# Performance work log

Measured on AMD Instinct MI355X. Metric: run time of the kernel, lower is better.

## Reference

```python
import jax, jax.numpy as jnp
import numpy as np

H = 16        # num_attention_heads
DH = 64       # attention_head_dim
D = H * DH    # model dim = 1024
FF = 4 * D    # feed-forward inner dim = 4096
SCALE = DH ** -0.5
EPS = 1e-12


def _ln(x, g, b):
    m = jnp.mean(x, axis=-1, keepdims=True)
    v = jnp.mean((x - m) ** 2, axis=-1, keepdims=True)
    return (x - m) * jax.lax.rsqrt(v + EPS) * g + b


def _attn(x, ctx, Wq, Wk, Wv, Wo, bo, mask):
    # x: [B,S,D] (already pre-normed), ctx: [B,T,D], mask: [B,T] int (1=keep) or None
    B, S, _ = x.shape
    T = ctx.shape[1]
    q = (x @ Wq).reshape(B, S, H, DH)
    k = (ctx @ Wk).reshape(B, T, H, DH)
    v = (ctx @ Wv).reshape(B, T, H, DH)
    scores = jnp.einsum('bqhd,bkhd->bhqk', q, k) * SCALE  # [B,H,S,T]
    if mask is not None:
        scores = jnp.where(mask[:, None, None, :] == 0, -jnp.inf, scores)
    probs = jax.nn.softmax(scores, axis=-1)
    out = jnp.einsum('bhqk,bkhd->bqhd', probs, v).reshape(B, S, D)
    return out @ Wo + bo


def _geglu_ff(x, Wff1, bff1, Wff2, bff2):
    y = x @ Wff1 + bff1                 # [B,S,2*FF]
    h, gate = y[..., :FF], y[..., FF:]
    # GEGLU computes exact (erf) gelu in fp32
    g = jax.nn.gelu(gate.astype(jnp.float32), approximate=False).astype(gate.dtype)
    return (h * g) @ Wff2 + bff2


def setup_inputs() -> dict:
    key = jax.random.key(0)
    ks = jax.random.split(key, 24)
    B, S, T = 4, 1024, 1024
    w = lambda k, shp: jax.random.normal(k, shp, dtype=jnp.float32) * 0.02
    inp = {
        'hidden_states': jax.random.normal(ks[0], (B, S, D), dtype=jnp.float32),
        'context': jax.random.normal(ks[1], (B, T, D), dtype=jnp.float32),
        'encoder_key_padding_mask': jnp.ones((B, T), dtype=jnp.int32),
        'g1': jnp.ones((D,), jnp.float32), 'b1': jnp.zeros((D,), jnp.float32),
        'g2': jnp.ones((D,), jnp.float32), 'b2': jnp.zeros((D,), jnp.float32),
        'g3': jnp.ones((D,), jnp.float32), 'b3': jnp.zeros((D,), jnp.float32),
        'Wq1': w(ks[2], (D, D)), 'Wk1': w(ks[3], (D, D)), 'Wv1': w(ks[4], (D, D)),
        'Wo1': w(ks[5], (D, D)), 'bo1': jnp.zeros((D,), jnp.float32),
        'Wq2': w(ks[6], (D, D)), 'Wk2': w(ks[7], (D, D)), 'Wv2': w(ks[8], (D, D)),
        'Wo2': w(ks[9], (D, D)), 'bo2': jnp.zeros((D,), jnp.float32),
        'Wff1': w(ks[10], (D, 2 * FF)), 'bff1': jnp.zeros((2 * FF,), jnp.float32),
        'Wff2': w(ks[11], (FF, D)), 'bff2': jnp.zeros((D,), jnp.float32),
    }
    return inp


def reference(hidden_states, context, encoder_key_padding_mask,
              g1, b1, g2, b2, g3, b3,
              Wq1, Wk1, Wv1, Wo1, bo1,
              Wq2, Wk2, Wv2, Wo2, bo2,
              Wff1, bff1, Wff2, bff2):
    # Self-attention (attn1): context defaults to (normed) hidden_states, no padding mask
    n1 = _ln(hidden_states, g1, b1)
    h = hidden_states + _attn(n1, n1, Wq1, Wk1, Wv1, Wo1, bo1, None)
    # Cross-attention (attn2) with encoder key padding mask
    n2 = _ln(h, g2, b2)
    h = h + _attn(n2, context, Wq2, Wk2, Wv2, Wo2, bo2, encoder_key_padding_mask)
    # GEGLU feed-forward
    h = h + _geglu_ff(_ln(h, g3, b3), Wff1, bff1, Wff2, bff2)
    return h
```

## Files before the change

### kernel.cpp

```cpp
#include <hip/hip_runtime.h>

typedef unsigned short u16;
typedef unsigned int u32;

#define B_ 4
#define S_ 1024
#define D_ 1024
#define H_ 16
#define DH_ 64
#define FF_ 4096
#define M_ 4096
#define SCALE_ 0.125f

typedef __attribute__((ext_vector_type(8))) __bf16 bf16x8;
typedef __attribute__((ext_vector_type(4))) float f32x4;

__device__ __forceinline__ f32x4 mfma16(bf16x8 a, bf16x8 b, f32x4 c) {
  return __builtin_amdgcn_mfma_f32_16x16x32_bf16(a, b, c, 0, 0, 0);
}

__device__ __forceinline__ u16 f2bf(float x) {
  union { __bf16 h; u16 u; } cv; cv.h = (__bf16)x; return cv.u;
}
__device__ __forceinline__ float bf2f(u16 u) {
  union { u32 u; float f; } cv; cv.u = ((u32)u) << 16; return cv.f;
}
__device__ __forceinline__ u32 packbf2(float a, float b) {
  union { u32 u; __bf16 h[2]; } pk;
  pk.h[0] = (__bf16)a; pk.h[1] = (__bf16)b;
  return pk.u;
}
__device__ __forceinline__ float gelu_exact(float x) {
  return 0.5f * x * (1.f + erff(x * 0.7071067811865475f));
}
__device__ __forceinline__ void gload16(const void* g, void* l) {
  __builtin_amdgcn_global_load_lds((__attribute__((address_space(1))) void*)(g),
                                   (__attribute__((address_space(3))) void*)(l),
                                   16, 0, 0);
}

template<int EPI>
__global__ __launch_bounds__(256, 2) void gemm128(
    const u16* __restrict__ A, const u16* __restrict__ BT,
    const float* __restrict__ bias, const float* __restrict__ res,
    const u16* __restrict__ aux, void* __restrict__ out,
    int M, int N, int K, int ktiles)
{
  __shared__ u16 As[2][128 * 64];
  __shared__ u16 Bs[2][128 * 64];

  const int tid = threadIdx.x;
  const int wave = tid >> 6, lane = tid & 63;
  const int wm = wave >> 1, wn = wave & 1;
  const int qi = lane & 15, g = lane >> 4;

  const int gx = N >> 7;
  const int nwg = gx * (M >> 7);
  int id = blockIdx.y * gridDim.x + blockIdx.x;
  id = (id & 7) * (nwg >> 3) + (id >> 3);
  const int m0 = (id / gx) << 7, n0 = (id % gx) << 7;

  const int NT = ktiles;
  const int kbase = blockIdx.z * ktiles * 64;

  const int r0 = tid >> 3;
  const int scol = (((tid & 7) ^ ((tid >> 3) & 7)) << 3);
  const int swb = wave << 6;

  f32x4 acc[4][4];
#pragma unroll
  for (int i = 0; i < 4; ++i)
#pragma unroll
    for (int j = 0; j < 4; ++j)
      acc[i][j] = (f32x4){0.f, 0.f, 0.f, 0.f};

#define STAGE_A(t, h, b) {                                                  \
    const int tt = (t) >= NT ? (t) - NT : (t);                              \
    _Pragma("unroll")                                                       \
    for (int i = 0; i < 2; ++i) {                                           \
      const int r = (h) * 64 + i * 32 + r0;                                 \
      gload16(A + (size_t)(m0 + r) * K + kbase + tt * 64 + scol,            \
              &As[b][(h) * 4096 + (i * 256 + swb) * 8]);                    \
    } }
#define STAGE_B(t, h, b) {                                                  \
    const int tt = (t) >= NT ? (t) - NT : (t);                              \
    _Pragma("unroll")                                                       \
    for (int i = 0; i < 2; ++i) {                                           \
      const int r = (h) * 64 + i * 32 + r0;                                 \
      gload16(BT + (size_t)(n0 + r) * K + kbase + tt * 64 + scol,           \
              &Bs[b][(h) * 4096 + (i * 256 + swb) * 8]);                    \
    } }

  bf16x8 af[4][2], bfr[4][2];

#define RD_ALL(b)                                                            \
  _Pragma("unroll") for (int mi = 0; mi < 4; ++mi)                           \
  _Pragma("unroll") for (int kk = 0; kk < 2; ++kk) {                         \
    const int row = wm * 64 + mi * 16 + qi;                                  \
    const int cb = ((kk * 64 + (g << 4)) ^ ((qi & 7) << 4));                 \
    af[mi][kk] = *(const bf16x8*)((const char*)&As[b][0] + row * 128 + cb);  \
  }                                                                          \
  _Pragma("unroll") for (int ni = 0; ni < 4; ++ni)                           \
  _Pragma("unroll") for (int kk = 0; kk < 2; ++kk) {                         \
    const int row = wn * 64 + ni * 16 + qi;                                  \
    const int cb = ((kk * 64 + (g << 4)) ^ ((qi & 7) << 4));                 \
    bfr[ni][kk] = *(const bf16x8*)((const char*)&Bs[b][0] + row * 128 + cb); \
  }

#define HALF(milo)                                                           \
  _Pragma("unroll") for (int mi = (milo); mi < (milo) + 2; ++mi)             \
  _Pragma("unroll") for (int ni = 0; ni < 4; ++ni)                           \
  _Pragma("unroll") for (int kk = 0; kk < 2; ++kk)                           \
    acc[mi][ni] = mfma16(af[mi][kk], bfr[ni][kk], acc[mi][ni]);

#define BAR() __builtin_amdgcn_s_barrier()
#define LGKM0() { asm volatile("s_waitcnt lgkmcnt(0)" ::: "memory");         \
                  __builtin_amdgcn_sched_barrier(0); }
#define VM8() asm volatile("s_waitcnt vmcnt(8)" ::: "memory")
#define PRIO(x) __builtin_amdgcn_s_setprio(x)

  STAGE_A(0, 0, 0); STAGE_A(0, 1, 0); STAGE_B(0, 0, 0); STAGE_B(0, 1, 0);
  STAGE_A(1, 0, 1); STAGE_A(1, 1, 1); STAGE_B(1, 0, 1); STAGE_B(1, 1, 1);
  VM8();
  BAR();

  const int NI = NT >> 1;
  for (int it = 0; it < NI; ++it) {
    const int k = it * 2;
    RD_ALL(0); LGKM0();
    BAR();
    STAGE_A(k + 2, 0, 0); STAGE_A(k + 2, 1, 0);
    PRIO(1); HALF(0); PRIO(0);
    STAGE_B(k + 2, 0, 0); STAGE_B(k + 2, 1, 0);
    PRIO(1); HALF(2); PRIO(0);
    VM8();
    BAR();
    RD_ALL(1); LGKM0();
    BAR();
    STAGE_A(k + 3, 0, 1); STAGE_A(k + 3, 1, 1);
    PRIO(1); HALF(0); PRIO(0);
    STAGE_B(k + 3, 0, 1); STAGE_B(k + 3, 1, 1);
    PRIO(1); HALF(2); PRIO(0);
    VM8();
    BAR();
  }

#pragma unroll
  for (int mi = 0; mi < 4; ++mi) {
#pragma unroll
    for (int ni = 0; ni < 4; ++ni) {
#pragma unroll
      for (int r = 0; r < 4; ++r) {
        const int m = m0 + wm * 64 + mi * 16 + g * 4 + r;
        const int n = n0 + wn * 64 + ni * 16 + qi;
        float v = acc[mi][ni][r];
        if (EPI == 0 || EPI == 5) {
          const int ts = n >> 10, b = m >> 10, s = m & 1023;
          const int hh = (n >> 6) & 15, dh = n & 63;
          if (EPI == 0 && ts == 0) v *= SCALE_;
          ((u16*)out)[(size_t)ts * (B_ * H_ * S_ * DH_) +
                      (((size_t)(b * H_ + hh) * S_) + s) * DH_ + dh] = f2bf(v);
        } else if (EPI == 1) {
          const size_t idx = (size_t)m * N + n;
          ((float*)out)[idx] = res[idx] + v + bias[n];
        } else if (EPI == 2) {
          ((u16*)out)[(size_t)m * N + n] = f2bf(gelu_exact(v + bias[n]));
        } else if (EPI == 3) {
          const size_t idx = (size_t)m * N + n;
          ((u16*)out)[idx] = f2bf((v + bias[n]) * bf2f(aux[idx]));
        } else {
          const size_t idx = (size_t)blockIdx.z * ((size_t)M * N) +
                             (size_t)m * N + n;
          ((u16*)out)[idx] = f2bf(v);
        }
      }
    }
  }
#undef STAGE_A
#undef STAGE_B
#undef RD_ALL
#undef HALF
#undef BAR
#undef LGKM0
#undef VM8
#undef PRIO
}

template<int EPI>
__global__ __launch_bounds__(512, 2) void gemm256b(
    const u16* __restrict__ A, const u16* __restrict__ BT,
    const float* __restrict__ bias, const float* __restrict__ res,
    const u16* __restrict__ aux, void* __restrict__ out,
    int M, int N, int K, int ktiles)
{
  __shared__ u16 As[2][256 * 64];
  __shared__ u16 Bs[2][256 * 64];

  const int tid = threadIdx.x;
  const int wave = tid >> 6, lane = tid & 63;
  const int wm = wave >> 2, wn = wave & 3;
  const int qi = lane & 15, g = lane >> 4;

  const int gx = N >> 8;
  const int nwg = gx * (M >> 8);
  int id = blockIdx.y * gridDim.x + blockIdx.x;
  id = (id & 7) * (nwg >> 3) + (id >> 3);
  const int m0 = (id / gx) << 8, n0 = (id % gx) << 8;

  const int NT = ktiles;
  const int kbase = blockIdx.z * ktiles * 64;

  const int srow = tid >> 3;
  const int scol = (((tid & 7) ^ ((tid >> 3) & 7)) << 3);
  const int sldsb = wave << 9;

  f32x4 acc[8][4];
#pragma unroll
  for (int i = 0; i < 8; ++i)
#pragma unroll
    for (int j = 0; j < 4; ++j)
      acc[i][j] = (f32x4){0.f, 0.f, 0.f, 0.f};

#define STAGE_A(t, b) {                                                     \
    const int tt = (t) >= NT ? (t) - NT : (t);                              \
    _Pragma("unroll")                                                       \
    for (int i = 0; i < 4; ++i) {                                           \
      const int r = i * 64 + srow;                                          \
      gload16(A + (size_t)(m0 + r) * K + kbase + tt * 64 + scol,            \
              &As[b][i * 4096 + sldsb]);                                    \
    } }
#define STAGE_B(t, b) {                                                     \
    const int tt = (t) >= NT ? (t) - NT : (t);                              \
    _Pragma("unroll")                                                       \
    for (int i = 0; i < 4; ++i) {                                           \
      const int r = i * 64 + srow;                                          \
      gload16(BT + (size_t)(n0 + r) * K + kbase + tt * 64 + scol,           \
              &Bs[b][i * 4096 + sldsb]);                                    \
    } }

  bf16x8 af[8][2], bfr[4][2];

#define RD_ALL(b)                                                            \
  _Pragma("unroll") for (int mi = 0; mi < 8; ++mi)                           \
  _Pragma("unroll") for (int kk = 0; kk < 2; ++kk) {                         \
    const int row = wm * 128 + mi * 16 + qi;                                 \
    const int cb = ((kk * 64 + (g << 4)) ^ ((qi & 7) << 4));                 \
    af[mi][kk] = *(const bf16x8*)((const char*)&As[b][0] + row * 128 + cb);  \
  }                                                                          \
  _Pragma("unroll") for (int ni = 0; ni < 4; ++ni)                           \
  _Pragma("unroll") for (int kk = 0; kk < 2; ++kk) {                         \
    const int row = wn * 64 + ni * 16 + qi;                                  \
    const int cb = ((kk * 64 + (g << 4)) ^ ((qi & 7) << 4));                 \
    bfr[ni][kk] = *(const bf16x8*)((const char*)&Bs[b][0] + row * 128 + cb); \
  }

#define MHALF(milo)                                                          \
  _Pragma("unroll") for (int mi = (milo); mi < (milo) + 4; ++mi)             \
  _Pragma("unroll") for (int ni = 0; ni < 4; ++ni)                           \
  _Pragma("unroll") for (int kk = 0; kk < 2; ++kk)                           \
    acc[mi][ni] = mfma16(af[mi][kk], bfr[ni][kk], acc[mi][ni]);

#define BAR() __builtin_amdgcn_s_barrier()
#define LGKM0() { asm volatile("s_waitcnt lgkmcnt(0)" ::: "memory");         \
                  __builtin_amdgcn_sched_barrier(0); }
#define VM8() asm volatile("s_waitcnt vmcnt(8)" ::: "memory")
#define PRIO(x) __builtin_amdgcn_s_setprio(x)

  STAGE_A(0, 0); STAGE_B(0, 0);
  STAGE_A(1, 1); STAGE_B(1, 1);
  VM8();
  BAR();

  for (int t = 0; t < NT; ++t) {
    const int b = t & 1;
    RD_ALL(b); LGKM0();
    BAR();
    STAGE_A(t + 2, b);
    PRIO(1); MHALF(0); PRIO(0);
    STAGE_B(t + 2, b);
    PRIO(1); MHALF(4); PRIO(0);
    VM8();
    BAR();
  }

#pragma unroll
  for (int mi = 0; mi < 8; ++mi) {
#pragma unroll
    for (int ni = 0; ni < 4; ++ni) {
#pragma unroll
      for (int r = 0; r < 4; ++r) {
        const int m = m0 + wm * 128 + mi * 16 + g * 4 + r;
        const int n = n0 + wn * 64 + ni * 16 + qi;
        const float v = acc[mi][ni][r];
        if (EPI == 2) {
          ((u16*)out)[(size_t)m * N + n] = f2bf(gelu_exact(v + bias[n]));
        } else if (EPI == 3) {
          const size_t idx = (size_t)m * N + n;
          ((u16*)out)[idx] = f2bf((v + bias[n]) * bf2f(aux[idx]));
        } else {
          const size_t idx = (size_t)blockIdx.z * ((size_t)M * N) +
                             (size_t)m * N + n;
          ((u16*)out)[idx] = f2bf(v);
        }
      }
    }
  }
#undef STAGE_A
#undef STAGE_B
#undef RD_ALL
#undef MHALF
#undef BAR
#undef LGKM0
#undef VM8
#undef PRIO
}

template<bool DOLN, int NS>
__global__ __launch_bounds__(256) void reduce_ln(
    const u16* __restrict__ p, const float* __restrict__ bias,
    const float* __restrict__ res, float* __restrict__ outf,
    const float* __restrict__ gg, const float* __restrict__ bb,
    u16* __restrict__ outn)
{
  __shared__ float red[8];
  const int row = blockIdx.x, tid = threadIdx.x;
  const size_t base = (size_t)row * 1024 + tid * 4;
  const size_t total = (size_t)M_ * 1024;
  float a0 = 0.f, a1 = 0.f, a2 = 0.f, a3 = 0.f;
#pragma unroll
  for (int s = 0; s < NS; ++s) {
    const uint2 u = *(const uint2*)&p[(size_t)s * total + base];
    a0 += bf2f((u16)(u.x & 0xffff));
    a1 += bf2f((u16)(u.x >> 16));
    a2 += bf2f((u16)(u.y & 0xffff));
    a3 += bf2f((u16)(u.y >> 16));
  }
  const float4 b4 = ((const float4*)bias)[tid];
  const float4 r4 = *(const float4*)&res[base];
  float4 o;
  o.x = r4.x + a0 + b4.x;
  o.y = r4.y + a1 + b4.y;
  o.z = r4.z + a2 + b4.z;
  o.w = r4.w + a3 + b4.w;
  *(float4*)&outf[base] = o;

  if (DOLN) {
    float s1 = o.x + o.y + o.z + o.w;
    float s2 = o.x * o.x + o.y * o.y + o.z * o.z + o.w * o.w;
#pragma unroll
    for (int m = 32; m; m >>= 1) {
      s1 += __shfl_xor(s1, m);
      s2 += __shfl_xor(s2, m);
    }
    const int wave = tid >> 6, lane = tid & 63;
    if (lane == 0) { red[wave * 2] = s1; red[wave * 2 + 1] = s2; }
    __syncthreads();
    const float St = red[0] + red[2] + red[4] + red[6];
    const float SQt = red[1] + red[3] + red[5] + red[7];
    const float mean = St * (1.f / 1024.f);
    float var = SQt * (1.f / 1024.f) - mean * mean;
    var = fmaxf(var, 0.f);
    const float rinv = rsqrtf(var + 1e-12f);
    const float4 g4 = ((const float4*)gg)[tid];
    const float4 bb4 = ((const float4*)bb)[tid];
    uint2 w;
    w.x = packbf2((o.x - mean) * rinv * g4.x + bb4.x,
                  (o.y - mean) * rinv * g4.y + bb4.y);
    w.y = packbf2((o.z - mean) * rinv * g4.z + bb4.z,
                  (o.w - mean) * rinv * g4.w + bb4.w);
    ((uint2*)(outn + (size_t)row * 1024))[tid] = w;
  }
}

template<int NS, bool QSC>
__global__ __launch_bounds__(256) void reduce_perm(
    const u16* __restrict__ p, u16* __restrict__ out, int M, int N)
{
  const size_t flat = ((size_t)blockIdx.x * 256 + threadIdx.x) * 4;
  const size_t total = (size_t)M * N;
  float a0 = 0.f, a1 = 0.f, a2 = 0.f, a3 = 0.f;
#pragma unroll
  for (int s = 0; s < NS; ++s) {
    const uint2 u = *(const uint2*)&p[(size_t)s * total + flat];
    a0 += bf2f((u16)(u.x & 0xffff));
    a1 += bf2f((u16)(u.x >> 16));
    a2 += bf2f((u16)(u.y & 0xffff));
    a3 += bf2f((u16)(u.y >> 16));
  }
  if (QSC) { a0 *= SCALE_; a1 *= SCALE_; a2 *= SCALE_; a3 *= SCALE_; }
  const int m = (int)(flat / N), nb = (int)(flat % N);
  const int ts = nb >> 10, hh = (nb >> 6) & 15, dh = nb & 63;
  const int b = m >> 10, sI = m & 1023;
  uint2 w;
  w.x = packbf2(a0, a1);
  w.y = packbf2(a2, a3);
  *(uint2*)&out[(size_t)ts * (B_ * H_ * S_ * DH_) +
                (((size_t)(b * H_ + hh) * S_) + sI) * DH_ + dh] = w;
}

template<bool MASKED>
__global__ __launch_bounds__(256, 4) void attn_kernel(
    const u16* __restrict__ Q, const u16* __restrict__ Kb,
    const u16* __restrict__ VT, const float* __restrict__ bias,
    u16* __restrict__ O, int S, int T)
{
  __shared__ u16 Ks[64 * 72];
  __shared__ u16 VTs[64 * 72];
  __shared__ u16 Ps[4][16 * 72];
  __shared__ float biasS[64];

  const int bh = blockIdx.y;
  const int b = bh >> 4, h = bh & 15;
  const int tid = threadIdx.x;
  const int wave = tid >> 6, lane = tid & 63;
  const int g = lane >> 4, qi = lane & 15;
  const int q0w = blockIdx.x * 64 + wave * 16;

  const u16* Qb = Q + (size_t)bh * S * DH_;
  const u16* Kg = Kb + (size_t)bh * T * DH_;
  const u16* Vg = VT + (size_t)bh * DH_ * T;

  bf16x8 qf[2];
  qf[0] = *(const bf16x8*)&Qb[(q0w + qi) * DH_ + g * 8];
  qf[1] = *(const bf16x8*)&Qb[(q0w + qi) * DH_ + 32 + g * 8];

  f32x4 acc[4];
#pragma unroll
  for (int i = 0; i < 4; ++i) acc[i] = (f32x4){0.f, 0.f, 0.f, 0.f};
  float l_run = 1e-30f;

  u16* Pw = &Ps[wave][0];

  for (int t0 = 0; t0 < T; t0 += 64) {
    __syncthreads();
#pragma unroll
    for (int i = 0; i < 2; ++i) {
      const int flat = i * 256 + tid;
      const int row = flat >> 3, kc = flat & 7;
      *(uint4*)&Ks[row * 72 + kc * 8] = *(const uint4*)&Kg[(size_t)(t0 + row) * DH_ + kc * 8];
      *(uint4*)&VTs[row * 72 + kc * 8] = *(const uint4*)&Vg[(size_t)row * T + t0 + kc * 8];
    }
    if (MASKED && tid < 64) biasS[tid] = bias[b * T + t0 + tid];
    __syncthreads();

    f32x4 sacc[4];
#pragma unroll
    for (int nt = 0; nt < 4; ++nt) sacc[nt] = (f32x4){0.f, 0.f, 0.f, 0.f};
#pragma unroll
    for (int kk = 0; kk < 2; ++kk) {
#pragma unroll
      for (int nt = 0; nt < 4; ++nt) {
        bf16x8 kf = *(const bf16x8*)&Ks[(nt * 16 + qi) * 72 + kk * 32 + g * 8];
        sacc[nt] = mfma16(kf, qf[kk], sacc[nt]);
      }
    }
    float p[4][4];
    float lsum = 0.f;
#pragma unroll
    for (int nt = 0; nt < 4; ++nt)
#pragma unroll
      for (int r = 0; r < 4; ++r) {
        float v = sacc[nt][r];
        if (MASKED) v += biasS[nt * 16 + g * 4 + r];
        const float e = __expf(v);
        p[nt][r] = e;
        lsum += e;
      }
    lsum += __shfl_xor(lsum, 16);
    lsum += __shfl_xor(lsum, 32);
    l_run += lsum;

#pragma unroll
    for (int nt = 0; nt < 4; ++nt) {
      uint2 w;
      w.x = packbf2(p[nt][0], p[nt][1]);
      w.y = packbf2(p[nt][2], p[nt][3]);
      *(uint2*)&Pw[qi * 72 + nt * 16 + g * 4] = w;
    }

#pragma unroll
    for (int kk = 0; kk < 2; ++kk) {
      bf16x8 pf = *(const bf16x8*)&Pw[qi * 72 + kk * 32 + g * 8];
#pragma unroll
      for (int ndh = 0; ndh < 4; ++ndh) {
        bf16x8 vf = *(const bf16x8*)&VTs[(ndh * 16 + qi) * 72 + kk * 32 + g * 8];
        acc[ndh] = mfma16(vf, pf, acc[ndh]);
      }
    }
  }

  const float inv = 1.f / l_run;
  const int qg = q0w + qi;
#pragma unroll
  for (int ndh = 0; ndh < 4; ++ndh) {
    uint2 w;
    w.x = packbf2(acc[ndh][0] * inv, acc[ndh][1] * inv);
    w.y = packbf2(acc[ndh][2] * inv, acc[ndh][3] * inv);
    *(uint2*)&O[(size_t)(b * S_ + qg) * D_ + h * DH_ + ndh * 16 + g * 4] = w;
  }
}

__global__ __launch_bounds__(256) void ln_kernel(
    const float* __restrict__ x, const float* __restrict__ gg,
    const float* __restrict__ bb, u16* __restrict__ out)
{
  __shared__ float red[8];
  const int row = blockIdx.x, tid = threadIdx.x;
  const float4 v = ((const float4*)(x + (size_t)row * D_))[tid];
  float s = v.x + v.y + v.z + v.w;
  float sq = v.x * v.x + v.y * v.y + v.z * v.z + v.w * v.w;
#pragma unroll
  for (int m = 32; m; m >>= 1) {
    s += __shfl_xor(s, m);
    sq += __shfl_xor(sq, m);
  }
  const int wave = tid >> 6, lane = tid & 63;
  if (lane == 0) { red[wave * 2] = s; red[wave * 2 + 1] = sq; }
  __syncthreads();
  const float St = red[0] + red[2] + red[4] + red[6];
  const float SQt = red[1] + red[3] + red[5] + red[7];
  const float mean = St * (1.f / 1024.f);
  float var = SQt * (1.f / 1024.f) - mean * mean;
  var = fmaxf(var, 0.f);
  const float rinv = rsqrtf(var + 1e-12f);
  const float4 g4 = ((const float4*)gg)[tid];
  const float4 b4 = ((const float4*)bb)[tid];
  uint2 o;
  o.x = packbf2((v.x - mean) * rinv * g4.x + b4.x, (v.y - mean) * rinv * g4.y + b4.y);
  o.y = packbf2((v.z - mean) * rinv * g4.z + b4.z, (v.w - mean) * rinv * g4.w + b4.w);
  ((uint2*)(out + (size_t)row * D_))[tid] = o;
}

__global__ __launch_bounds__(256) void transpose_w(
    const float* __restrict__ in, u16* __restrict__ out, int K, int N)
{
  __shared__ float tile[32][33];
  const int tx = threadIdx.x & 31, ty = threadIdx.x >> 5;
  const int k0 = blockIdx.y * 32, n0 = blockIdx.x * 32;
#pragma unroll
  for (int j = 0; j < 4; ++j)
    tile[ty + 8 * j][tx] = in[(size_t)(k0 + ty + 8 * j) * N + n0 + tx];
  __syncthreads();
#pragma unroll
  for (int j = 0; j < 4; ++j)
    out[(size_t)(n0 + ty + 8 * j) * K + k0 + tx] = f2bf(tile[tx][ty + 8 * j]);
}

__global__ __launch_bounds__(256) void transpose_v(
    const u16* __restrict__ in, u16* __restrict__ out, int T)
{
  __shared__ u16 tile[32][33];
  const int tx = threadIdx.x & 31, ty = threadIdx.x >> 5;
  const int bh = blockIdx.z;
  const int t0 = blockIdx.x * 32, d0 = blockIdx.y * 32;
  const u16* ib = in + (size_t)bh * T * DH_;
  u16* ob = out + (size_t)bh * DH_ * T;
#pragma unroll
  for (int j = 0; j < 4; ++j)
    tile[ty + 8 * j][tx] = ib[(size_t)(t0 + ty + 8 * j) * DH_ + d0 + tx];
  __syncthreads();
#pragma unroll
  for (int j = 0; j < 4; ++j)
    ob[(size_t)(d0 + ty + 8 * j) * T + t0 + tx] = tile[tx][ty + 8 * j];
}

__global__ void cvt_bf16(const float* __restrict__ in, u16* __restrict__ out, int n4)
{
  const int i = blockIdx.x * blockDim.x + threadIdx.x;
  if (i < n4) {
    const float4 v = ((const float4*)in)[i];
    uint2 o;
    o.x = packbf2(v.x, v.y);
    o.y = packbf2(v.z, v.w);
    ((uint2*)out)[i] = o;
  }
}

__global__ void mask_bias(const int* __restrict__ mask, float* __restrict__ bias, int n)
{
  const int i = blockIdx.x * blockDim.x + threadIdx.x;
  if (i < n) bias[i] = mask[i] ? 0.f : -1e30f;
}

extern "C" void kernel_launch(void* const* d_in, const int* in_sizes, int n_in,
                              void* d_out, int out_size, void* d_ws, size_t ws_size,
                              hipStream_t stream)
{
  (void)in_sizes; (void)n_in; (void)out_size; (void)ws_size;
  const float* hidden = (const float*)d_in[0];
  const float* ctx    = (const float*)d_in[1];
  const int*   mask   = (const int*)d_in[2];
  const float* g1 = (const float*)d_in[3];
  const float* b1 = (const float*)d_in[4];
  const float* g2 = (const float*)d_in[5];
  const float* b2 = (const float*)d_in[6];
  const float* g3 = (const float*)d_in[7];
  const float* b3 = (const float*)d_in[8];
  const float* Wq1 = (const float*)d_in[9];
  const float* Wk1 = (const float*)d_in[10];
  const float* Wv1 = (const float*)d_in[11];
  const float* Wo1 = (const float*)d_in[12];
  const float* bo1 = (const float*)d_in[13];
  const float* Wq2 = (const float*)d_in[14];
  const float* Wk2 = (const float*)d_in[15];
  const float* Wv2 = (const float*)d_in[16];
  const float* Wo2 = (const float*)d_in[17];
  const float* bo2 = (const float*)d_in[18];
  const float* Wff1 = (const float*)d_in[19];
  const float* bff1 = (const float*)d_in[20];
  const float* Wff2 = (const float*)d_in[21];
  const float* bff2 = (const float*)d_in[22];

  char* ws = (char*)d_ws;
  size_t off = 0;
  auto alloc = [&](size_t bytes) -> void* {
    void* p = ws + off;
    off += (bytes + 255) & ~(size_t)255;
    return p;
  };
  u16* WqT1  = (u16*)alloc((size_t)1024 * 1024 * 2);
  u16* WkT1  = (u16*)alloc((size_t)1024 * 1024 * 2);
  u16* WvT1  = (u16*)alloc((size_t)1024 * 1024 * 2);
  u16* WoT1  = (u16*)alloc((size_t)1024 * 1024 * 2);
  u16* WqT2  = (u16*)alloc((size_t)1024 * 1024 * 2);
  u16* WkT2  = (u16*)alloc((size_t)1024 * 1024 * 2);
  u16* WvT2  = (u16*)alloc((size_t)1024 * 1024 * 2);
  u16* WoT2  = (u16*)alloc((size_t)1024 * 1024 * 2);
  u16* Wff1T = (u16*)alloc((size_t)8192 * 1024 * 2);
  u16* Wff2T = (u16*)alloc((size_t)1024 * 4096 * 2);
  u16* nbuf  = (u16*)alloc((size_t)M_ * D_ * 2);
  u16* hgbuf = (u16*)alloc((size_t)M_ * FF_ * 2);
  u16* qbuf  = (u16*)alloc((size_t)M_ * D_ * 2);
  u16* kbuf  = (u16*)alloc((size_t)M_ * D_ * 2);
  u16* vbuf  = (u16*)alloc((size_t)M_ * D_ * 2);
  u16* vtbuf = (u16*)alloc((size_t)M_ * D_ * 2);
  u16* attnb = (u16*)alloc((size_t)M_ * D_ * 2);
  u16* ctxb  = (u16*)alloc((size_t)M_ * D_ * 2);
  u16* pbuf  = (u16*)alloc((size_t)4 * M_ * D_ * 2);
  float* biasw = (float*)alloc((size_t)B_ * S_ * 4);
  u16* gbuf = qbuf;
  float* hres = (float*)d_out;

  const dim3 blk(256);
  const dim3 blk512(512);
  const dim3 gW(32, 32);
  const dim3 gQKV(24, 32);
  const dim3 gKV(16, 32);
  const dim3 gFFb(16, 16);
  const dim3 gF2b(4, 16, 4);
  const dim3 gS2(8, 32, 2);
  const dim3 gA(16, 64);
  const dim3 gV(32, 2, 64);
  const dim3 gR(4096);

  transpose_w<<<gW, blk, 0, stream>>>(Wq1, WqT1, 1024, 1024);
  transpose_w<<<gW, blk, 0, stream>>>(Wk1, WkT1, 1024, 1024);
  transpose_w<<<gW, blk, 0, stream>>>(Wv1, WvT1, 1024, 1024);
  transpose_w<<<gW, blk, 0, stream>>>(Wo1, WoT1, 1024, 1024);
  transpose_w<<<gW, blk, 0, stream>>>(Wq2, WqT2, 1024, 1024);
  transpose_w<<<gW, blk, 0, stream>>>(Wk2, WkT2, 1024, 1024);
  transpose_w<<<gW, blk, 0, stream>>>(Wv2, WvT2, 1024, 1024);
  transpose_w<<<gW, blk, 0, stream>>>(Wo2, WoT2, 1024, 1024);
  transpose_w<<<dim3(256, 32), blk, 0, stream>>>(Wff1, Wff1T, 1024, 8192);
  transpose_w<<<dim3(32, 128), blk, 0, stream>>>(Wff2, Wff2T, 4096, 1024);
  cvt_bf16<<<dim3((1048576 + 255) / 256), blk, 0, stream>>>(ctx, ctxb, 1048576);
  mask_bias<<<dim3(16), blk, 0, stream>>>(mask, biasw, B_ * S_);

  ln_kernel<<<dim3(M_), blk, 0, stream>>>(hidden, g1, b1, nbuf);
  gemm128<0><<<gQKV, blk, 0, stream>>>(nbuf, WqT1, nullptr, nullptr, nullptr,
                                       qbuf, M_, 3072, 1024, 16);
  transpose_v<<<gV, blk, 0, stream>>>(vbuf, vtbuf, 1024);
  attn_kernel<false><<<gA, blk, 0, stream>>>(qbuf, kbuf, vtbuf, nullptr, attnb, S_, S_);
  gemm128<4><<<gS2, blk, 0, stream>>>(attnb, WoT1, nullptr, nullptr, nullptr,
                                      pbuf, M_, 1024, 1024, 8);
  reduce_ln<true, 2><<<gR, blk, 0, stream>>>(pbuf, bo1, hidden, hres, g2, b2, nbuf);

  gemm128<4><<<gS2, blk, 0, stream>>>(nbuf, WqT2, nullptr, nullptr, nullptr,
                                      pbuf, M_, 1024, 1024, 8);
  reduce_perm<2, true><<<gR, blk, 0, stream>>>(pbuf, qbuf, M_, 1024);
  gemm128<5><<<gKV, blk, 0, stream>>>(ctxb, WkT2, nullptr, nullptr, nullptr,
                                      kbuf, M_, 2048, 1024, 16);
  transpose_v<<<gV, blk, 0, stream>>>(vbuf, vtbuf, 1024);
  attn_kernel<true><<<gA, blk, 0, stream>>>(qbuf, kbuf, vtbuf, biasw, attnb, S_, S_);
  gemm128<4><<<gS2, blk, 0, stream>>>(attnb, WoT2, nullptr, nullptr, nullptr,
                                      pbuf, M_, 1024, 1024, 8);
  reduce_ln<true, 2><<<gR, blk, 0, stream>>>(pbuf, bo2, hres, hres, g3, b3, nbuf);

  gemm256b<2><<<gFFb, blk512, 0, stream>>>(nbuf, Wff1T + (size_t)FF_ * 1024,
                                           bff1 + FF_, nullptr, nullptr, gbuf,
                                           M_, FF_, 1024, 16);
  gemm256b<3><<<gFFb, blk512, 0, stream>>>(nbuf, Wff1T, bff1, nullptr, gbuf,
                                           hgbuf, M_, FF_, 1024, 16);
  gemm256b<4><<<gF2b, blk512, 0, stream>>>(hgbuf, Wff2T, nullptr, nullptr, nullptr,
                                           pbuf, M_, 1024, 4096, 16);
  reduce_ln<false, 4><<<gR, blk, 0, stream>>>(pbuf, bff2, hres, hres, nullptr,
                                              nullptr, nullptr);
}
```

Before: 403.9 us.

## Restructure 256x256 GEMM main loop into quadrant-wise interleaved load/compute pipeline

Replaces the FF GEMM's loop, which read all A/B fragments and then ran two MFMA halves, with an 8-phase schedule per pair of k-tiles. Each phase reads a quadrant of fragments, issues half-tile global->LDS loads for the next tiles, and runs a 4x2 MFMA quadrant between barriers. Fragment registers shrink (af from 8x2 to 4x2), and global loads are spread more finely across the compute. In exchange there are many more barriers per tile, and the loop assumes an even ktile count.

```diff
diff --git a/kernel.cpp b/kernel.cpp
--- a/kernel.cpp
+++ b/kernel.cpp
@@ -187,7 +187,7 @@
 }
 
 template<int EPI>
-__global__ __launch_bounds__(512, 2) void gemm256b(
+__global__ __launch_bounds__(512, 2) void gemm256p(
     const u16* __restrict__ A, const u16* __restrict__ BT,
     const float* __restrict__ bias, const float* __restrict__ res,
     const u16* __restrict__ aux, void* __restrict__ out,
@@ -221,66 +221,85 @@
     for (int j = 0; j < 4; ++j)
       acc[i][j] = (f32x4){0.f, 0.f, 0.f, 0.f};
 
-#define STAGE_A(t, b) {                                                     \
+#define SA(t, h, b) {                                                       \
     const int tt = (t) >= NT ? (t) - NT : (t);                              \
     _Pragma("unroll")                                                       \
-    for (int i = 0; i < 4; ++i) {                                           \
-      const int r = i * 64 + srow;                                          \
+    for (int i = 0; i < 2; ++i) {                                           \
+      const int r = (h) * 128 + i * 64 + srow;                              \
       gload16(A + (size_t)(m0 + r) * K + kbase + tt * 64 + scol,            \
-              &As[b][i * 4096 + sldsb]);                                    \
+              &As[b][(h) * 8192 + i * 4096 + sldsb]);                       \
     } }
-#define STAGE_B(t, b) {                                                     \
+#define SB(t, h, b) {                                                       \
     const int tt = (t) >= NT ? (t) - NT : (t);                              \
     _Pragma("unroll")                                                       \
-    for (int i = 0; i < 4; ++i) {                                           \
-      const int r = i * 64 + srow;                                          \
+    for (int i = 0; i < 2; ++i) {                                           \
+      const int r = (h) * 128 + i * 64 + srow;                              \
       gload16(BT + (size_t)(n0 + r) * K + kbase + tt * 64 + scol,           \
-              &Bs[b][i * 4096 + sldsb]);                                    \
+              &Bs[b][(h) * 8192 + i * 4096 + sldsb]);                       \
     } }
 
-  bf16x8 af[8][2], bfr[4][2];
-
-#define RD_ALL(b)                                                            \
-  _Pragma("unroll") for (int mi = 0; mi < 8; ++mi)                           \
+  bf16x8 af[4][2], bfr[4][2];
+
+#define RD_A(b, mq)                                                          \
+  _Pragma("unroll") for (int mi = 0; mi < 4; ++mi)                           \
   _Pragma("unroll") for (int kk = 0; kk < 2; ++kk) {                         \
-    const int row = wm * 128 + mi * 16 + qi;                                 \
+    const int row = wm * 128 + (mq) * 64 + mi * 16 + qi;                     \
     const int cb = ((kk * 64 + (g << 4)) ^ ((qi & 7) << 4));                 \
     af[mi][kk] = *(const bf16x8*)((const char*)&As[b][0] + row * 128 + cb);  \
-  }                                                                          \
-  _Pragma("unroll") for (int ni = 0; ni < 4; ++ni)                           \
+  }
+#define RD_B(b, nq)                                                          \
+  _Pragma("unroll") for (int ni = 0; ni < 2; ++ni)                           \
   _Pragma("unroll") for (int kk = 0; kk < 2; ++kk) {                         \
-    const int row = wn * 64 + ni * 16 + qi;                                  \
+    const int row = wn * 64 + (nq) * 32 + ni * 16 + qi;                      \
     const int cb = ((kk * 64 + (g << 4)) ^ ((qi & 7) << 4));                 \
-    bfr[ni][kk] = *(const bf16x8*)((const char*)&Bs[b][0] + row * 128 + cb); \
-  }
-
-#define MHALF(milo)                                                          \
-  _Pragma("unroll") for (int mi = (milo); mi < (milo) + 4; ++mi)             \
-  _Pragma("unroll") for (int ni = 0; ni < 4; ++ni)                           \
+    bfr[(nq) * 2 + ni][kk] =                                                 \
+        *(const bf16x8*)((const char*)&Bs[b][0] + row * 128 + cb);           \
+  }
+#define QUAD(mq, nq)                                                         \
+  _Pragma("unroll") for (int mi = 0; mi < 4; ++mi)                           \
+  _Pragma("unroll") for (int ni = 0; ni < 2; ++ni)                           \
   _Pragma("unroll") for (int kk = 0; kk < 2; ++kk)                           \
-    acc[mi][ni] = mfma16(af[mi][kk], bfr[ni][kk], acc[mi][ni]);
+    acc[(mq) * 4 + mi][(nq) * 2 + ni] =                                      \
+        mfma16(af[mi][kk], bfr[(nq) * 2 + ni][kk],                           \
+               acc[(mq) * 4 + mi][(nq) * 2 + ni]);
 
 #define BAR() __builtin_amdgcn_s_barrier()
 #define LGKM0() { asm volatile("s_waitcnt lgkmcnt(0)" ::: "memory");         \
                   __builtin_amdgcn_sched_barrier(0); }
-#define VM8() asm volatile("s_waitcnt vmcnt(8)" ::: "memory")
+#define VM4() asm volatile("s_waitcnt vmcnt(4)" ::: "memory")
 #define PRIO(x) __builtin_amdgcn_s_setprio(x)
 
-  STAGE_A(0, 0); STAGE_B(0, 0);
-  STAGE_A(1, 1); STAGE_B(1, 1);
-  VM8();
+  SA(0, 0, 0); SA(0, 1, 0); SB(0, 0, 0); SB(0, 1, 0);
+  SB(1, 0, 1); SB(1, 1, 1);
+  VM4();
   BAR();
 
-  for (int t = 0; t < NT; ++t) {
-    const int b = t & 1;
-    RD_ALL(b); LGKM0();
-    BAR();
-    STAGE_A(t + 2, b);
-    PRIO(1); MHALF(0); PRIO(0);
-    STAGE_B(t + 2, b);
-    PRIO(1); MHALF(4); PRIO(0);
-    VM8();
-    BAR();
+  const int NI = NT >> 1;
+  for (int it = 0; it < NI; ++it) {
+    const int t0 = it * 2, t1 = t0 + 1;
+    RD_A(0, 0); RD_B(0, 0); SA(t1, 0, 1);
+    BAR(); LGKM0(); PRIO(1); QUAD(0, 0); PRIO(0); BAR();
+
+    RD_B(0, 1); SA(t1, 1, 1);
+    BAR(); LGKM0(); PRIO(1); QUAD(0, 1); PRIO(0); BAR();
+
+    RD_A(0, 1); SB(t0 + 2, 0, 0);
+    BAR(); LGKM0(); PRIO(1); QUAD(1, 0); PRIO(0); BAR();
+
+    SB(t0 + 2, 1, 0);
+    BAR(); PRIO(1); QUAD(1, 1); PRIO(0); VM4(); BAR();
+
+    RD_A(1, 0); RD_B(1, 0); SA(t0 + 2, 0, 0);
+    BAR(); LGKM0(); PRIO(1); QUAD(0, 0); PRIO(0); BAR();
+
+    RD_B(1, 1); SA(t0 + 2, 1, 0);
+    BAR(); LGKM0(); PRIO(1); QUAD(0, 1); PRIO(0); BAR();
+
+    RD_A(1, 1); SB(t1 + 2, 0, 1);
+    BAR(); LGKM0(); PRIO(1); QUAD(1, 0); PRIO(0); BAR();
+
+    SB(t1 + 2, 1, 1);
+    BAR(); PRIO(1); QUAD(1, 1); PRIO(0); VM4(); BAR();
   }
 
 #pragma unroll
@@ -305,13 +324,14 @@
       }
     }
   }
-#undef STAGE_A
-#undef STAGE_B
-#undef RD_ALL
-#undef MHALF
+#undef SA
+#undef SB
+#undef RD_A
+#undef RD_B
+#undef QUAD
 #undef BAR
 #undef LGKM0
-#undef VM8
+#undef VM4
 #undef PRIO
 }
 
@@ -646,8 +666,8 @@
   const dim3 gW(32, 32);
   const dim3 gQKV(24, 32);
   const dim3 gKV(16, 32);
-  const dim3 gFFb(16, 16);
-  const dim3 gF2b(4, 16, 4);
+  const dim3 gFFp(16, 16);
+  const dim3 gF2p(4, 16, 4);
   const dim3 gS2(8, 32, 2);
   const dim3 gA(16, 64);
   const dim3 gV(32, 2, 64);
@@ -686,12 +706,12 @@
                                       pbuf, M_, 1024, 1024, 8);
   reduce_ln<true, 2><<<gR, blk, 0, stream>>>(pbuf, bo2, hres, hres, g3, b3, nbuf);
 
-  gemm256b<2><<<gFFb, blk512, 0, stream>>>(nbuf, Wff1T + (size_t)FF_ * 1024,
+  gemm256p<2><<<gFFp, blk512, 0, stream>>>(nbuf, Wff1T + (size_t)FF_ * 1024,
                                            bff1 + FF_, nullptr, nullptr, gbuf,
                                            M_, FF_, 1024, 16);
-  gemm256b<3><<<gFFb, blk512, 0, stream>>>(nbuf, Wff1T, bff1, nullptr, gbuf,
+  gemm256p<3><<<gFFp, blk512, 0, stream>>>(nbuf, Wff1T, bff1, nullptr, gbuf,
                                            hgbuf, M_, FF_, 1024, 16);
-  gemm256b<4><<<gF2b, blk512, 0, stream>>>(hgbuf, Wff2T, nullptr, nullptr, nullptr,
+  gemm256p<4><<<gF2p, blk512, 0, stream>>>(hgbuf, Wff2T, nullptr, nullptr, nullptr,
                                            pbuf, M_, 1024, 4096, 16);
   reduce_ln<false, 4><<<gR, blk, 0, stream>>>(pbuf, bff2, hres, hres, nullptr,
                                               nullptr, nullptr);
```

New measurement: 412.4 us. 2.1% more time.
